# Performance work log

Measured on AMD Instinct MI355X. Metric: run time of the kernel, lower is better.

## Reference

```python
import jax, jax.numpy as jnp
import numpy as np
from jax import lax

L, B, T, H, K, R = 2, 32, 2048, 512, 64, 7


def setup_inputs() -> dict:
    key = jax.random.key(0)
    ks = jax.random.split(key, 12)
    s = 1.0 / np.sqrt(H)
    sk = 1.0 / np.sqrt(1 * R)
    spa = 1.0 / np.sqrt(K)
    return {
        "hidden": jax.random.normal(ks[0], (L, B, H), jnp.float32),
        "encoder_output": jax.random.normal(ks[1], (T, B, H), jnp.float32),
        "enc_len": jax.random.randint(ks[2], (B,), 1, T + 1, jnp.int32),
        "prev_attention": jax.random.uniform(ks[3], (B, T), jnp.float32),
        "conv_w": jax.random.uniform(ks[4], (K, 1, R), jnp.float32, -sk, sk),
        "conv_b": jax.random.uniform(ks[5], (K,), jnp.float32, -sk, sk),
        "hp_w": jax.random.uniform(ks[6], (H, H), jnp.float32, -s, s),
        "hp_b": jax.random.uniform(ks[7], (H,), jnp.float32, -s, s),
        "pa_w": jax.random.uniform(ks[8], (H, K), jnp.float32, -spa, spa),
        "pa_b": jax.random.uniform(ks[9], (H,), jnp.float32, -spa, spa),
        "out_w": jax.random.uniform(ks[10], (1, H), jnp.float32, -s, s),
        "out_b": jax.random.uniform(ks[11], (1,), jnp.float32, -s, s),
    }


def reference(hidden, encoder_output, enc_len, prev_attention,
              conv_w, conv_b, hp_w, hp_b, pa_w, pa_b, out_w, out_b):
    # encoder_output: (T,B,H) -> (B,T,H)
    enc = jnp.transpose(encoder_output, (1, 0, 2))
    # bmm with uniform addMask == mean over decoder layers -> (B,1,H)
    h = jnp.mean(hidden, axis=0)[:, None, :]
    hidden_attn = h @ hp_w.T + hp_b                      # (B,1,H)
    # Conv1d(1,K,7,padding=3) on prev attention: (B,1,T) -> (B,K,T)
    x = prev_attention[:, None, :]
    y = lax.conv_general_dilated(x, conv_w, (1,), [(3, 3)],
                                 dimension_numbers=("NCH", "OIH", "NCH"))
    y = y + conv_b[None, :, None]
    conv_prev = jnp.transpose(y, (0, 2, 1)) @ pa_w.T + pa_b   # (B,T,H)
    res = jnp.tanh(enc + hidden_attn + conv_prev)             # (B,T,H)
    energy = (res @ out_w.T + out_b)[..., 0]                  # (B,T)
    # ragged masked softmax over valid positions per sample
    mask = jnp.arange(T)[None, :] < enc_len[:, None]
    w = jax.nn.softmax(jnp.where(mask, energy, -1e30), axis=1)
    w = jnp.where(mask, w, 0.0)
    return w[:, :, None]                                      # (B,T,1)
```

## Files before the change

### kernel.cpp

```cpp
#include <hip/hip_runtime.h>
#include <math.h>

#define L_ 2
#define B_ 32
#define T_ 2048
#define H_ 512
#define K_ 64
#define R_ 7
#define TT 64

__device__ __forceinline__ float tanh_fast(float x) {
    float e = __expf(2.0f * x);
    return 1.0f - 2.0f * __builtin_amdgcn_rcpf(e + 1.0f);
}

__global__ void prep_ha(const float* __restrict__ hidden,
                        const float* __restrict__ hp_w,
                        const float* __restrict__ hp_b,
                        float* __restrict__ ha) {
    __shared__ float hm[4][H_];
    const int b0 = blockIdx.y * 4;
    const int h0 = blockIdx.x * 256;
    const int tid = threadIdx.x;
    for (int i = tid; i < 4 * H_; i += 256) {
        int bb = i >> 9, j = i & (H_ - 1);
        hm[bb][j] = 0.5f * (hidden[(0 * B_ + b0 + bb) * H_ + j] +
                            hidden[(1 * B_ + b0 + bb) * H_ + j]);
    }
    __syncthreads();
    const int h = h0 + tid;
    const float4* row = (const float4*)(hp_w + (size_t)h * H_);
    float acc0 = 0.f, acc1 = 0.f, acc2 = 0.f, acc3 = 0.f;
    for (int j4 = 0; j4 < H_ / 4; ++j4) {
        float4 w = row[j4];
        int j = j4 * 4;
        acc0 = fmaf(w.x, hm[0][j], fmaf(w.y, hm[0][j+1], fmaf(w.z, hm[0][j+2], fmaf(w.w, hm[0][j+3], acc0))));
        acc1 = fmaf(w.x, hm[1][j], fmaf(w.y, hm[1][j+1], fmaf(w.z, hm[1][j+2], fmaf(w.w, hm[1][j+3], acc1))));
        acc2 = fmaf(w.x, hm[2][j], fmaf(w.y, hm[2][j+1], fmaf(w.z, hm[2][j+2], fmaf(w.w, hm[2][j+3], acc2))));
        acc3 = fmaf(w.x, hm[3][j], fmaf(w.y, hm[3][j+1], fmaf(w.z, hm[3][j+2], fmaf(w.w, hm[3][j+3], acc3))));
    }
    float hb = hp_b[h];
    ha[(b0 + 0) * H_ + h] = acc0 + hb;
    ha[(b0 + 1) * H_ + h] = acc1 + hb;
    ha[(b0 + 2) * H_ + h] = acc2 + hb;
    ha[(b0 + 3) * H_ + h] = acc3 + hb;
}

__global__ void prep_w2(const float* __restrict__ pa_w,
                        const float* __restrict__ pa_b,
                        const float* __restrict__ conv_w,
                        const float* __restrict__ conv_b,
                        float* __restrict__ w2t,
                        float* __restrict__ c2) {
    const int h = blockIdx.x * 256 + threadIdx.x;
    float wr[R_];
#pragma unroll
    for (int r = 0; r < R_; ++r) wr[r] = 0.f;
    float cb = 0.f;
    for (int k = 0; k < K_; ++k) {
        float pw = pa_w[h * K_ + k];
        cb = fmaf(pw, conv_b[k], cb);
#pragma unroll
        for (int r = 0; r < R_; ++r) wr[r] = fmaf(pw, conv_w[k * R_ + r], wr[r]);
    }
#pragma unroll
    for (int r = 0; r < R_; ++r) w2t[r * H_ + h] = wr[r];
    c2[h] = cb + pa_b[h];
}

__global__ __launch_bounds__(256, 4) void energy_kernel(
    const float* __restrict__ enc,
    const float* __restrict__ prev_att,
    const int*   __restrict__ enc_len,
    const float* __restrict__ ha,
    const float* __restrict__ w2t,
    const float* __restrict__ c2,
    const float* __restrict__ out_w,
    const float* __restrict__ out_b,
    float* __restrict__ energy)
{
    const int b  = blockIdx.y;
    const int t0 = blockIdx.x * TT;
    const int len = enc_len[b];
    if (t0 >= len) return;

    const int tid  = threadIdx.x;
    const int lane = tid & 63;
    const int wave = tid >> 6;

    __shared__ float pa_s[TT + 6];
    for (int i = tid; i < TT + 6; i += 256) {
        int t = t0 - 3 + i;
        pa_s[i] = (t >= 0 && t < T_) ? prev_att[b * T_ + t] : 0.0f;
    }
    __syncthreads();

    const float4* haq = (const float4*)(ha + b * H_);
    const float4* c2q = (const float4*)c2;
    const float4* owq = (const float4*)out_w;
    float4 hacA = haq[lane];
    float4 hacB = haq[64 + lane];
    {
        float4 cA = c2q[lane], cB = c2q[64 + lane];
        hacA.x += cA.x; hacA.y += cA.y; hacA.z += cA.z; hacA.w += cA.w;
        hacB.x += cB.x; hacB.y += cB.y; hacB.z += cB.z; hacB.w += cB.w;
    }
    const float4 owA = owq[lane], owB = owq[64 + lane];
    float4 w2A[R_], w2B[R_];
#pragma unroll
    for (int r = 0; r < R_; ++r) {
        const float4* wq = (const float4*)(w2t + r * H_);
        w2A[r] = wq[lane];
        w2B[r] = wq[64 + lane];
    }
    const float ob = out_b[0];

    int t = t0 + wave * (TT / 4);
    const int tend = min(t + TT / 4, len);
    for (; t < tend; ++t) {
        const float4* e4 = (const float4*)(enc + ((size_t)t * B_ + b) * H_);
        float4 eA = e4[lane];
        float4 eB = e4[64 + lane];
        const int ti = t - t0;
        float4 cA = hacA, cB = hacB;
#pragma unroll
        for (int r = 0; r < R_; ++r) {
            float p = pa_s[ti + r];
            cA.x = fmaf(w2A[r].x, p, cA.x);
            cA.y = fmaf(w2A[r].y, p, cA.y);
            cA.z = fmaf(w2A[r].z, p, cA.z);
            cA.w = fmaf(w2A[r].w, p, cA.w);
            cB.x = fmaf(w2B[r].x, p, cB.x);
            cB.y = fmaf(w2B[r].y, p, cB.y);
            cB.z = fmaf(w2B[r].z, p, cB.z);
            cB.w = fmaf(w2B[r].w, p, cB.w);
        }
        float acc;
        acc  = owA.x * tanh_fast(eA.x + cA.x);
        acc += owA.y * tanh_fast(eA.y + cA.y);
        acc += owA.z * tanh_fast(eA.z + cA.z);
        acc += owA.w * tanh_fast(eA.w + cA.w);
        acc += owB.x * tanh_fast(eB.x + cB.x);
        acc += owB.y * tanh_fast(eB.y + cB.y);
        acc += owB.z * tanh_fast(eB.z + cB.z);
        acc += owB.w * tanh_fast(eB.w + cB.w);
#pragma unroll
        for (int off = 32; off > 0; off >>= 1)
            acc += __shfl_xor(acc, off);
        if (lane == 0) energy[b * T_ + t] = acc + ob;
    }
}

__global__ void softmax_kernel(float* __restrict__ energy_out,
                               const int* __restrict__ enc_len) {
    const int b   = blockIdx.x;
    const int tid = threadIdx.x;
    const int len = enc_len[b];
    __shared__ float sm[4];
    const int wave = tid >> 6, lane = tid & 63;

    float e[8];
    float m = -1e30f;
#pragma unroll
    for (int i = 0; i < 8; ++i) {
        int t = tid + i * 256;
        e[i] = energy_out[b * T_ + t];
        if (t < len) m = fmaxf(m, e[i]);
    }
#pragma unroll
    for (int off = 32; off > 0; off >>= 1)
        m = fmaxf(m, __shfl_xor(m, off));
    if (lane == 0) sm[wave] = m;
    __syncthreads();
    m = fmaxf(fmaxf(sm[0], sm[1]), fmaxf(sm[2], sm[3]));
    __syncthreads();

    float p[8];
    float s = 0.f;
#pragma unroll
    for (int i = 0; i < 8; ++i) {
        int t = tid + i * 256;
        p[i] = (t < len) ? __expf(e[i] - m) : 0.0f;
        s += p[i];
    }
#pragma unroll
    for (int off = 32; off > 0; off >>= 1)
        s += __shfl_xor(s, off);
    if (lane == 0) sm[wave] = s;
    __syncthreads();
    s = sm[0] + sm[1] + sm[2] + sm[3];
    const float inv = 1.0f / s;
#pragma unroll
    for (int i = 0; i < 8; ++i) {
        int t = tid + i * 256;
        energy_out[b * T_ + t] = p[i] * inv;
    }
}

extern "C" void kernel_launch(void* const* d_in, const int* in_sizes, int n_in,
                              void* d_out, int out_size, void* d_ws, size_t ws_size,
                              hipStream_t stream) {
    const float* hidden   = (const float*)d_in[0];
    const float* enc      = (const float*)d_in[1];
    const int*   enc_len  = (const int*)  d_in[2];
    const float* prev_att = (const float*)d_in[3];
    const float* conv_w   = (const float*)d_in[4];
    const float* conv_b   = (const float*)d_in[5];
    const float* hp_w     = (const float*)d_in[6];
    const float* hp_b     = (const float*)d_in[7];
    const float* pa_w     = (const float*)d_in[8];
    const float* pa_b     = (const float*)d_in[9];
    const float* out_w    = (const float*)d_in[10];
    const float* out_b    = (const float*)d_in[11];

    float* out = (float*)d_out;
    float* ws  = (float*)d_ws;
    float* ha  = ws;
    float* w2t = ha + B_ * H_;
    float* c2  = w2t + R_ * H_;

    prep_ha<<<dim3(2, 8), 256, 0, stream>>>(hidden, hp_w, hp_b, ha);
    prep_w2<<<2, 256, 0, stream>>>(pa_w, pa_b, conv_w, conv_b, w2t, c2);
    energy_kernel<<<dim3(T_ / TT, B_), 256, 0, stream>>>(
        enc, prev_att, enc_len, ha, w2t, c2, out_w, out_b, out);
    softmax_kernel<<<B_, 256, 0, stream>>>(out, enc_len);
}
```

Measured before the change: 244.6 us.

## Fuse prep kernels, halve energy tile, and prefetch next encoder row

Merges the two small weight-prep kernels into one launch, with block ranges choosing the role, and reads the shared hidden mean as float4. The energy kernel tile shrinks from 64 to 32 timesteps, doubling the grid for better load balance across ragged lengths. It also software-prefetches the next timestep's encoder row while computing the current one. The aim is to cut launch overhead and hide memory latency, at the cost of more registers and extra per-block setup loads.

```diff
diff --git a/kernel.cpp b/kernel.cpp
--- a/kernel.cpp
+++ b/kernel.cpp
@@ -7,65 +7,70 @@
 #define H_ 512
 #define K_ 64
 #define R_ 7
-#define TT 64
+#define TT 32
 
 __device__ __forceinline__ float tanh_fast(float x) {
     float e = __expf(2.0f * x);
     return 1.0f - 2.0f * __builtin_amdgcn_rcpf(e + 1.0f);
 }
 
-__global__ void prep_ha(const float* __restrict__ hidden,
-                        const float* __restrict__ hp_w,
-                        const float* __restrict__ hp_b,
-                        float* __restrict__ ha) {
+__global__ void prep_fused(const float* __restrict__ hidden,
+                           const float* __restrict__ hp_w,
+                           const float* __restrict__ hp_b,
+                           const float* __restrict__ pa_w,
+                           const float* __restrict__ pa_b,
+                           const float* __restrict__ conv_w,
+                           const float* __restrict__ conv_b,
+                           float* __restrict__ ha,
+                           float* __restrict__ w2t,
+                           float* __restrict__ c2) {
+    const int tid = threadIdx.x;
+    if (blockIdx.x >= 16) {
+        const int h = (blockIdx.x - 16) * 256 + tid;
+        float wr[R_];
+#pragma unroll
+        for (int r = 0; r < R_; ++r) wr[r] = 0.f;
+        float cb = 0.f;
+        for (int k = 0; k < K_; ++k) {
+            float pw = pa_w[h * K_ + k];
+            cb = fmaf(pw, conv_b[k], cb);
+#pragma unroll
+            for (int r = 0; r < R_; ++r) wr[r] = fmaf(pw, conv_w[k * R_ + r], wr[r]);
+        }
+#pragma unroll
+        for (int r = 0; r < R_; ++r) w2t[r * H_ + h] = wr[r];
+        c2[h] = cb + pa_b[h];
+        return;
+    }
     __shared__ float hm[4][H_];
-    const int b0 = blockIdx.y * 4;
-    const int h0 = blockIdx.x * 256;
-    const int tid = threadIdx.x;
+    const int b0 = (blockIdx.x >> 1) * 4;
+    const int h0 = (blockIdx.x & 1) * 256;
     for (int i = tid; i < 4 * H_; i += 256) {
         int bb = i >> 9, j = i & (H_ - 1);
-        hm[bb][j] = 0.5f * (hidden[(0 * B_ + b0 + bb) * H_ + j] +
-                            hidden[(1 * B_ + b0 + bb) * H_ + j]);
+        hm[bb][j] = 0.5f * (hidden[(b0 + bb) * H_ + j] +
+                            hidden[(B_ + b0 + bb) * H_ + j]);
     }
     __syncthreads();
     const int h = h0 + tid;
     const float4* row = (const float4*)(hp_w + (size_t)h * H_);
-    float acc0 = 0.f, acc1 = 0.f, acc2 = 0.f, acc3 = 0.f;
+    const float4* m0q = (const float4*)hm[0];
+    const float4* m1q = (const float4*)hm[1];
+    const float4* m2q = (const float4*)hm[2];
+    const float4* m3q = (const float4*)hm[3];
+    float a0 = 0.f, a1 = 0.f, a2 = 0.f, a3 = 0.f;
     for (int j4 = 0; j4 < H_ / 4; ++j4) {
-        float4 w = row[j4];
-        int j = j4 * 4;
-        acc0 = fmaf(w.x, hm[0][j], fmaf(w.y, hm[0][j+1], fmaf(w.z, hm[0][j+2], fmaf(w.w, hm[0][j+3], acc0))));
-        acc1 = fmaf(w.x, hm[1][j], fmaf(w.y, hm[1][j+1], fmaf(w.z, hm[1][j+2], fmaf(w.w, hm[1][j+3], acc1))));
-        acc2 = fmaf(w.x, hm[2][j], fmaf(w.y, hm[2][j+1], fmaf(w.z, hm[2][j+2], fmaf(w.w, hm[2][j+3], acc2))));
-        acc3 = fmaf(w.x, hm[3][j], fmaf(w.y, hm[3][j+1], fmaf(w.z, hm[3][j+2], fmaf(w.w, hm[3][j+3], acc3))));
+        float4 w  = row[j4];
+        float4 m0 = m0q[j4], m1 = m1q[j4], m2 = m2q[j4], m3 = m3q[j4];
+        a0 = fmaf(w.x, m0.x, fmaf(w.y, m0.y, fmaf(w.z, m0.z, fmaf(w.w, m0.w, a0))));
+        a1 = fmaf(w.x, m1.x, fmaf(w.y, m1.y, fmaf(w.z, m1.z, fmaf(w.w, m1.w, a1))));
+        a2 = fmaf(w.x, m2.x, fmaf(w.y, m2.y, fmaf(w.z, m2.z, fmaf(w.w, m2.w, a2))));
+        a3 = fmaf(w.x, m3.x, fmaf(w.y, m3.y, fmaf(w.z, m3.z, fmaf(w.w, m3.w, a3))));
     }
     float hb = hp_b[h];
-    ha[(b0 + 0) * H_ + h] = acc0 + hb;
-    ha[(b0 + 1) * H_ + h] = acc1 + hb;
-    ha[(b0 + 2) * H_ + h] = acc2 + hb;
-    ha[(b0 + 3) * H_ + h] = acc3 + hb;
-}
-
-__global__ void prep_w2(const float* __restrict__ pa_w,
-                        const float* __restrict__ pa_b,
-                        const float* __restrict__ conv_w,
-                        const float* __restrict__ conv_b,
-                        float* __restrict__ w2t,
-                        float* __restrict__ c2) {
-    const int h = blockIdx.x * 256 + threadIdx.x;
-    float wr[R_];
-#pragma unroll
-    for (int r = 0; r < R_; ++r) wr[r] = 0.f;
-    float cb = 0.f;
-    for (int k = 0; k < K_; ++k) {
-        float pw = pa_w[h * K_ + k];
-        cb = fmaf(pw, conv_b[k], cb);
-#pragma unroll
-        for (int r = 0; r < R_; ++r) wr[r] = fmaf(pw, conv_w[k * R_ + r], wr[r]);
-    }
-#pragma unroll
-    for (int r = 0; r < R_; ++r) w2t[r * H_ + h] = wr[r];
-    c2[h] = cb + pa_b[h];
+    ha[(b0 + 0) * H_ + h] = a0 + hb;
+    ha[(b0 + 1) * H_ + h] = a1 + hb;
+    ha[(b0 + 2) * H_ + h] = a2 + hb;
+    ha[(b0 + 3) * H_ + h] = a3 + hb;
 }
 
 __global__ __launch_bounds__(256, 4) void energy_kernel(
@@ -117,37 +122,46 @@
 
     int t = t0 + wave * (TT / 4);
     const int tend = min(t + TT / 4, len);
-    for (; t < tend; ++t) {
+    if (t < tend) {
         const float4* e4 = (const float4*)(enc + ((size_t)t * B_ + b) * H_);
         float4 eA = e4[lane];
         float4 eB = e4[64 + lane];
-        const int ti = t - t0;
-        float4 cA = hacA, cB = hacB;
-#pragma unroll
-        for (int r = 0; r < R_; ++r) {
-            float p = pa_s[ti + r];
-            cA.x = fmaf(w2A[r].x, p, cA.x);
-            cA.y = fmaf(w2A[r].y, p, cA.y);
-            cA.z = fmaf(w2A[r].z, p, cA.z);
-            cA.w = fmaf(w2A[r].w, p, cA.w);
-            cB.x = fmaf(w2B[r].x, p, cB.x);
-            cB.y = fmaf(w2B[r].y, p, cB.y);
-            cB.z = fmaf(w2B[r].z, p, cB.z);
-            cB.w = fmaf(w2B[r].w, p, cB.w);
+        for (; t < tend; ++t) {
+            float4 nA = eA, nB = eB;
+            if (t + 1 < tend) {
+                const float4* n4 = (const float4*)(enc + ((size_t)(t + 1) * B_ + b) * H_);
+                nA = n4[lane];
+                nB = n4[64 + lane];
+            }
+            const int ti = t - t0;
+            float4 cA = hacA, cB = hacB;
+#pragma unroll
+            for (int r = 0; r < R_; ++r) {
+                float p = pa_s[ti + r];
+                cA.x = fmaf(w2A[r].x, p, cA.x);
+                cA.y = fmaf(w2A[r].y, p, cA.y);
+                cA.z = fmaf(w2A[r].z, p, cA.z);
+                cA.w = fmaf(w2A[r].w, p, cA.w);
+                cB.x = fmaf(w2B[r].x, p, cB.x);
+                cB.y = fmaf(w2B[r].y, p, cB.y);
+                cB.z = fmaf(w2B[r].z, p, cB.z);
+                cB.w = fmaf(w2B[r].w, p, cB.w);
+            }
+            float acc;
+            acc  = owA.x * tanh_fast(eA.x + cA.x);
+            acc += owA.y * tanh_fast(eA.y + cA.y);
+            acc += owA.z * tanh_fast(eA.z + cA.z);
+            acc += owA.w * tanh_fast(eA.w + cA.w);
+            acc += owB.x * tanh_fast(eB.x + cB.x);
+            acc += owB.y * tanh_fast(eB.y + cB.y);
+            acc += owB.z * tanh_fast(eB.z + cB.z);
+            acc += owB.w * tanh_fast(eB.w + cB.w);
+#pragma unroll
+            for (int off = 32; off > 0; off >>= 1)
+                acc += __shfl_xor(acc, off);
+            if (lane == 0) energy[b * T_ + t] = acc + ob;
+            eA = nA; eB = nB;
         }
-        float acc;
-        acc  = owA.x * tanh_fast(eA.x + cA.x);
-        acc += owA.y * tanh_fast(eA.y + cA.y);
-        acc += owA.z * tanh_fast(eA.z + cA.z);
-        acc += owA.w * tanh_fast(eA.w + cA.w);
-        acc += owB.x * tanh_fast(eB.x + cB.x);
-        acc += owB.y * tanh_fast(eB.y + cB.y);
-        acc += owB.z * tanh_fast(eB.z + cB.z);
-        acc += owB.w * tanh_fast(eB.w + cB.w);
-#pragma unroll
-        for (int off = 32; off > 0; off >>= 1)
-            acc += __shfl_xor(acc, off);
-        if (lane == 0) energy[b * T_ + t] = acc + ob;
     }
 }
 
@@ -219,8 +233,8 @@
     float* w2t = ha + B_ * H_;
     float* c2  = w2t + R_ * H_;
 
-    prep_ha<<<dim3(2, 8), 256, 0, stream>>>(hidden, hp_w, hp_b, ha);
-    prep_w2<<<2, 256, 0, stream>>>(pa_w, pa_b, conv_w, conv_b, w2t, c2);
+    prep_fused<<<18, 256, 0, stream>>>(hidden, hp_w, hp_b, pa_w, pa_b,
+                                       conv_w, conv_b, ha, w2t, c2);
     energy_kernel<<<dim3(T_ / TT, B_), 256, 0, stream>>>(
         enc, prev_att, enc_len, ha, w2t, c2, out_w, out_b, out);
     softmax_kernel<<<B_, 256, 0, stream>>>(out, enc_len);
```

Measured after the change: 237.1 us. -3.1%, faster.
